# Performance work log

Hardware: AMD Instinct MI355X
Metric: run time of the kernel (lower is better)

## Reference

```python
import jax, jax.numpy as jnp
import numpy as np

B, S, D = 4, 2048, 1024  # batch, seq_len, input_dim == output_dim (dk)


def setup_inputs() -> dict:
    key = jax.random.key(0)
    kx, kq, kk, kv = jax.random.split(key, 4)
    # xavier_uniform bound for square [D, D] matrices
    bound = float(np.sqrt(6.0 / (D + D)))
    return {
        "x": jax.random.normal(kx, (B, S, D), dtype=jnp.float32),
        "WQ": jax.random.uniform(kq, (D, D), jnp.float32, -bound, bound),
        "WK": jax.random.uniform(kk, (D, D), jnp.float32, -bound, bound),
        "WV": jax.random.uniform(kv, (D, D), jnp.float32, -bound, bound),
    }


def reference(x, WQ, WK, WV):
    dk = WQ.shape[1]
    q = x @ WQ  # [B, S, dk]
    k = x @ WK
    v = x @ WV
    scores = jnp.einsum("bsd,btd->bst", q, k) / jnp.sqrt(jnp.asarray(dk, x.dtype))
    # causal mask: tril ones -> positions where mask==0 set to -inf
    s = x.shape[1]
    causal = jnp.tril(jnp.ones((s, s), dtype=bool))
    scores = jnp.where(causal[None, :, :], scores, jnp.asarray(-jnp.inf, x.dtype))
    attention = jax.nn.softmax(scores, axis=-1)
    # NOTE: original applies attention_dropout to `scores` post-softmax and
    # discards the result -> dead op; eval-mode output is attention @ v.
    return jnp.einsum("bst,btd->bsd", attention, v)
```

## Files before the change

kernel.cpp:

```cpp
#include <hip/hip_runtime.h>
#include <stdint.h>


typedef unsigned short u16;
typedef __attribute__((ext_vector_type(8))) short shortx8;
typedef __attribute__((ext_vector_type(4))) float floatx4;

static constexpr int BB = 4;
static constexpr int SS = 2048;
static constexpr int DD = 1024;

__device__ __forceinline__ u16 f2bf(float f) {
  union { float f; uint32_t u; } c; c.f = f;
  uint32_t u = c.u;
  return (u16)((u + 0x7fffu + ((u >> 16) & 1u)) >> 16);
}

__device__ __forceinline__ float bfhi2f(uint32_t u) {
  union { uint32_t u; float f; } c; c.u = u & 0xffff0000u; return c.f;
}
__device__ __forceinline__ float bflo2f(uint32_t u) {
  union { uint32_t u; float f; } c; c.u = u << 16; return c.f;
}

#define GLOAD_LDS16(g_, l_)                                                             \
  __builtin_amdgcn_global_load_lds((const __attribute__((address_space(1))) void*)(g_), \
                                   (__attribute__((address_space(3))) void*)(l_), 16, 0, 0)

__device__ __forceinline__ void gemm_core_128(
    const u16* __restrict__ A, const u16* __restrict__ Bt,
    int lda, int ldb, int m0, int n0, int kend, floatx4 acc[4][4])
{
  __shared__ u16 lA[128 * 64];
  __shared__ u16 lB[128 * 64];
  const int t = threadIdx.x;
  const int w = t >> 6, l = t & 63;
  const int wm = w >> 1, wn = w & 1;
  const int sr = l >> 3;
  const int scq = ((l & 7) ^ (l >> 3)) * 8;

#pragma unroll
  for (int i = 0; i < 4; ++i)
#pragma unroll
    for (int j = 0; j < 4; ++j)
      acc[i][j] = (floatx4){0.f, 0.f, 0.f, 0.f};

  const u16* Ab = A + (size_t)m0 * lda;
  const u16* Bb = Bt + (size_t)n0 * ldb;

  for (int k0 = 0; k0 < kend; k0 += 64) {
#pragma unroll
    for (int i = 0; i < 4; ++i) {
      const int row = w * 32 + i * 8;
      GLOAD_LDS16(Ab + (size_t)(row + sr) * lda + k0 + scq, &lA[row * 64]);
      GLOAD_LDS16(Bb + (size_t)(row + sr) * ldb + k0 + scq, &lB[row * 64]);
    }
    __syncthreads();

#pragma unroll
    for (int ks = 0; ks < 2; ++ks) {
      const int ca = ((ks * 4 + (l >> 4)) ^ (l & 7)) * 8;
      shortx8 af[4], bf[4];
#pragma unroll
      for (int i = 0; i < 4; ++i)
        af[i] = *(const shortx8*)&lA[(wm * 64 + i * 16 + (l & 15)) * 64 + ca];
#pragma unroll
      for (int i = 0; i < 4; ++i)
        bf[i] = *(const shortx8*)&lB[(wn * 64 + i * 16 + (l & 15)) * 64 + ca];
#pragma unroll
      for (int i = 0; i < 4; ++i)
#pragma unroll
        for (int j = 0; j < 4; ++j)
          acc[i][j] = __builtin_amdgcn_mfma_f32_16x16x32_bf16(af[i], bf[j], acc[i][j], 0, 0, 0);
    }
    __syncthreads();
  }
}

#define LOAD_AF(mh_)                                                                     \
  _Pragma("unroll")                                                                      \
  for (int mi = 0; mi < 4; ++mi)                                                         \
    _Pragma("unroll")                                                                    \
    for (int kk = 0; kk < 2; ++kk)                                                       \
      af[mi][kk] = *(const shortx8*)&As[((mh_) * 128 + wr * 64 + mi * 16 + fr) * 64 +    \
                                        (((kk * 4 + fq) ^ (l & 7)) * 8)];

#define LOAD_BF(nh_)                                                                     \
  _Pragma("unroll")                                                                      \
  for (int ni = 0; ni < 2; ++ni)                                                         \
    _Pragma("unroll")                                                                    \
    for (int kk = 0; kk < 2; ++kk)                                                       \
      bf[ni][kk] = *(const shortx8*)&Bs[((nh_) * 128 + wc * 32 + ni * 16 + fr) * 64 +    \
                                        (((kk * 4 + fq) ^ (l & 7)) * 8)];

#define MFMA_QUAD(mh_, nh_)                                                              \
  do {                                                                                   \
    __builtin_amdgcn_s_setprio(1);                                                       \
    _Pragma("unroll")                                                                    \
    for (int mi = 0; mi < 4; ++mi)                                                       \
      _Pragma("unroll")                                                                  \
      for (int ni = 0; ni < 2; ++ni)                                                     \
        _Pragma("unroll")                                                                \
        for (int kk = 0; kk < 2; ++kk)                                                   \
          acc[mh_][nh_][mi][ni] = __builtin_amdgcn_mfma_f32_16x16x32_bf16(               \
              af[mi][kk], bf[ni][kk], acc[mh_][nh_][mi][ni], 0, 0, 0);                   \
    __builtin_amdgcn_s_setprio(0);                                                       \
  } while (0)

#define STAGE_A(buf_, half_, k_)                                                         \
  do {                                                                                   \
    _Pragma("unroll")                                                                    \
    for (int j = 0; j < 2; ++j) {                                                        \
      const int row0 = (half_) * 128 + wv * 16 + j * 8;                                  \
      GLOAD_LDS16(Ab + (size_t)(row0 + sr) * lda + (k_) + scq, &sm[buf_][0][row0 * 64]); \
    }                                                                                    \
  } while (0)

#define STAGE_B(buf_, half_, k_)                                                         \
  do {                                                                                   \
    _Pragma("unroll")                                                                    \
    for (int j = 0; j < 2; ++j) {                                                        \
      const int row0 = (half_) * 128 + wv * 16 + j * 8;                                  \
      GLOAD_LDS16(Bb + (size_t)(row0 + sr) * ldb + (k_) + scq, &sm[buf_][1][row0 * 64]); \
    }                                                                                    \
  } while (0)

__device__ __forceinline__ void gemm_core_256(
    const u16* __restrict__ A, const u16* __restrict__ Bt,
    int lda, int ldb, int m0, int n0, int kend,
    floatx4 (&acc)[2][2][4][2])
{
  __shared__ u16 sm[2][2][256 * 64];
  const int t = threadIdx.x;
  const int wv = t >> 6, l = t & 63;
  const int wr = wv >> 2, wc = wv & 3;
  const int fr = l & 15, fq = l >> 4;
  const int sr = l >> 3;
  const int scq = ((l & 7) ^ sr) * 8;

#pragma unroll
  for (int a = 0; a < 2; ++a)
#pragma unroll
    for (int bq = 0; bq < 2; ++bq)
#pragma unroll
      for (int mi = 0; mi < 4; ++mi)
#pragma unroll
        for (int ni = 0; ni < 2; ++ni)
          acc[a][bq][mi][ni] = (floatx4){0.f, 0.f, 0.f, 0.f};

  const u16* Ab = A + (size_t)m0 * lda;
  const u16* Bb = Bt + (size_t)n0 * ldb;
  const int T = kend >> 6;

  STAGE_A(0, 0, 0); STAGE_A(0, 1, 0);
  STAGE_B(0, 0, 0); STAGE_B(0, 1, 0);
  {
    const int k1p = (T > 1) ? 64 : 0;
    STAGE_A(1, 0, k1p);
    STAGE_B(1, 1, k1p);
  }
  asm volatile("s_waitcnt vmcnt(4)" ::: "memory");
  __builtin_amdgcn_s_barrier();

  shortx8 af[4][2], bf[2][2];

  for (int tt = 0; tt < T; ++tt) {
    const int c = tt & 1, o = c ^ 1;
    const u16* As = &sm[c][0][0];
    const u16* Bs = &sm[c][1][0];
    const int kn1 = ((tt + 1 < T) ? tt + 1 : T - 1) * 64;
    const int kn2 = ((tt + 2 < T) ? tt + 2 : T - 1) * 64;

    LOAD_AF(0); LOAD_BF(0);
    STAGE_A(o, 1, kn1);
    __builtin_amdgcn_s_barrier();
    asm volatile("s_waitcnt lgkmcnt(0)" ::: "memory");
    MFMA_QUAD(0, 0);
    __builtin_amdgcn_s_barrier();

    LOAD_BF(1);
    STAGE_B(o, 0, kn1);
    __builtin_amdgcn_s_barrier();
    asm volatile("s_waitcnt lgkmcnt(0)" ::: "memory");
    MFMA_QUAD(0, 1);
    __builtin_amdgcn_s_barrier();

    LOAD_AF(1);
    STAGE_A(c, 0, kn2);
    __builtin_amdgcn_s_barrier();
    asm volatile("s_waitcnt lgkmcnt(0)" ::: "memory");
    MFMA_QUAD(1, 1);
    __builtin_amdgcn_s_barrier();

    LOAD_BF(0);
    STAGE_B(c, 1, kn2);
    __builtin_amdgcn_s_barrier();
    asm volatile("s_waitcnt lgkmcnt(0)" ::: "memory");
    MFMA_QUAD(1, 0);
    asm volatile("s_waitcnt vmcnt(4)" ::: "memory");
    __builtin_amdgcn_s_barrier();
  }
  asm volatile("s_waitcnt vmcnt(0)" ::: "memory");
}

__global__ __launch_bounds__(256) void prep(const float* __restrict__ x,
                                            const float* __restrict__ WQ,
                                            const float* __restrict__ WK,
                                            const float* __restrict__ WV,
                                            u16* __restrict__ xb,
                                            u16* __restrict__ Wt) {
  __shared__ float tile[64][65];
  const int bid = blockIdx.x;
  const int t = threadIdx.x;
  if (bid < 8192) {
    const size_t i = (size_t)bid * 256 + t;
    float4 v = ((const float4*)x)[i];
    ushort4 o;
    o.x = f2bf(v.x); o.y = f2bf(v.y); o.z = f2bf(v.z); o.w = f2bf(v.w);
    ((ushort4*)xb)[i] = o;
    return;
  }
  const int r = bid - 8192;
  const int wsel = r >> 8;
  const int rr = r & 255;
  const int k0 = (rr >> 4) * 64, n0 = (rr & 15) * 64;
  const float* W = wsel == 0 ? WQ : (wsel == 1 ? WK : WV);
  const int tx = t & 63, ty = t >> 6;
#pragma unroll
  for (int i = 0; i < 16; ++i)
    tile[ty + i * 4][tx] = W[(size_t)(k0 + ty + i * 4) * DD + n0 + tx];
  __syncthreads();
  u16* dst = Wt + (size_t)wsel * DD * DD;
#pragma unroll
  for (int i = 0; i < 16; ++i)
    dst[(size_t)(n0 + ty + i * 4) * DD + k0 + tx] = f2bf(tile[tx][ty + i * 4]);
}

__global__ __launch_bounds__(512, 2) void qkv_gemm(const u16* __restrict__ x,
                                                   const u16* __restrict__ Wt,
                                                   u16* __restrict__ Q,
                                                   u16* __restrict__ K,
                                                   u16* __restrict__ Vt) {
  const int m0 = blockIdx.x * 256;
  const int n0t = blockIdx.y * 256;
  floatx4 acc[2][2][4][2];
  gemm_core_256(x, Wt, DD, DD, m0, n0t, DD, acc);

  const int t = threadIdx.x, wv = t >> 6, l = t & 63;
  const int wr = wv >> 2, wc = wv & 3;
  const int fr = l & 15, fq = l >> 4;

  if (n0t >= 2048) {
    const int bb = m0 >> 11;
    u16* vt = Vt + (size_t)bb * DD * SS;
    const int sb = m0 & 2047;
#pragma unroll
    for (int mh = 0; mh < 2; ++mh)
#pragma unroll
      for (int nh = 0; nh < 2; ++nh)
#pragma unroll
        for (int mi = 0; mi < 4; ++mi)
#pragma unroll
          for (int ni = 0; ni < 2; ++ni) {
            const int d = (n0t - 2048) + nh * 128 + wc * 32 + ni * 16 + fr;
            const int s = sb + mh * 128 + wr * 64 + mi * 16 + fq * 4;
            ushort4 o4;
            o4.x = f2bf(acc[mh][nh][mi][ni][0]);
            o4.y = f2bf(acc[mh][nh][mi][ni][1]);
            o4.z = f2bf(acc[mh][nh][mi][ni][2]);
            o4.w = f2bf(acc[mh][nh][mi][ni][3]);
            *(ushort4*)(vt + (size_t)d * SS + s) = o4;
          }
    return;
  }

  u16* out = (n0t < 1024) ? Q : K;
  const int n0 = n0t & 1023;
#pragma unroll
  for (int mh = 0; mh < 2; ++mh)
#pragma unroll
    for (int nh = 0; nh < 2; ++nh)
#pragma unroll
      for (int mi = 0; mi < 4; ++mi)
#pragma unroll
        for (int ni = 0; ni < 2; ++ni)
#pragma unroll
          for (int r = 0; r < 4; ++r) {
            const int m = m0 + mh * 128 + wr * 64 + mi * 16 + fq * 4 + r;
            const int n = n0 + nh * 128 + wc * 32 + ni * 16 + fr;
            out[(size_t)m * DD + n] = f2bf(acc[mh][nh][mi][ni][r]);
          }
}

__global__ __launch_bounds__(512, 2) void scores_gemm(const u16* __restrict__ Q,
                                                      const u16* __restrict__ Kt,
                                                      u16* __restrict__ Scb) {
  const int b = blockIdx.z;
  const int tcode = blockIdx.x;
  int mb = (int)((sqrtf(8.0f * (float)tcode + 1.0f) - 1.0f) * 0.5f);
  while ((mb + 1) * (mb + 2) / 2 <= tcode) ++mb;
  while (mb * (mb + 1) / 2 > tcode) --mb;
  const int nb = tcode - mb * (mb + 1) / 2;
  const int m0 = mb * 256, n0 = nb * 256;

  floatx4 acc[2][2][4][2];
  gemm_core_256(Q + (size_t)b * SS * DD, Kt + (size_t)b * SS * DD, DD, DD, m0, n0, DD, acc);

  u16* out = Scb + (size_t)b * SS * SS;
  const int t = threadIdx.x, wv = t >> 6, l = t & 63;
  const int wr = wv >> 2, wc = wv & 3;
  const int fr = l & 15, fq = l >> 4;
#pragma unroll
  for (int mh = 0; mh < 2; ++mh)
#pragma unroll
    for (int nh = 0; nh < 2; ++nh)
#pragma unroll
      for (int mi = 0; mi < 4; ++mi)
#pragma unroll
        for (int ni = 0; ni < 2; ++ni)
#pragma unroll
          for (int r = 0; r < 4; ++r) {
            const int m = m0 + mh * 128 + wr * 64 + mi * 16 + fq * 4 + r;
            const int n = n0 + nh * 128 + wc * 32 + ni * 16 + fr;
            out[(size_t)m * SS + n] = f2bf(acc[mh][nh][mi][ni][r] * 0.03125f);
          }
}

__global__ __launch_bounds__(256) void softmax_causal(const u16* __restrict__ Scb,
                                                      u16* __restrict__ P) {
  const int row = blockIdx.x * 4 + (threadIdx.x >> 6);
  const int l = threadIdx.x & 63;
  const int b = row >> 11, i = row & 2047;
  const u16* s = Scb + (size_t)b * SS * SS + (size_t)i * SS;
  u16* p = P + (size_t)b * SS * SS + (size_t)i * SS;
  const int n = i + 1;
  const int jend = (i + 128) & ~127;
  const int nc = (jend + 511) >> 9;

  float v[4][8];
  float mx = -INFINITY;
#pragma unroll
  for (int c = 0; c < 4; ++c) {
    if (c < nc) {
      const int col = c * 512 + l * 8;
      uint4 raw = *(const uint4*)(s + col);
      v[c][0] = bflo2f(raw.x); v[c][1] = bfhi2f(raw.x);
      v[c][2] = bflo2f(raw.y); v[c][3] = bfhi2f(raw.y);
      v[c][4] = bflo2f(raw.z); v[c][5] = bfhi2f(raw.z);
      v[c][6] = bflo2f(raw.w); v[c][7] = bfhi2f(raw.w);
#pragma unroll
      for (int e = 0; e < 8; ++e) {
        v[c][e] = (col + e < n) ? v[c][e] : -INFINITY;
        mx = fmaxf(mx, v[c][e]);
      }
    }
  }
#pragma unroll
  for (int o = 32; o > 0; o >>= 1) mx = fmaxf(mx, __shfl_xor(mx, o, 64));

  float sum = 0.f;
#pragma unroll
  for (int c = 0; c < 4; ++c) {
    if (c < nc) {
#pragma unroll
      for (int e = 0; e < 8; ++e) {
        v[c][e] = __expf(v[c][e] - mx);
        sum += v[c][e];
      }
    }
  }
#pragma unroll
  for (int o = 32; o > 0; o >>= 1) sum += __shfl_xor(sum, o, 64);
  const float inv = 1.0f / sum;

#pragma unroll
  for (int c = 0; c < 4; ++c) {
    if (c < nc) {
      const int col = c * 512 + l * 8;
      if (col < jend) {
        uint4 o4;
        o4.x = (uint32_t)f2bf(v[c][0] * inv) | ((uint32_t)f2bf(v[c][1] * inv) << 16);
        o4.y = (uint32_t)f2bf(v[c][2] * inv) | ((uint32_t)f2bf(v[c][3] * inv) << 16);
        o4.z = (uint32_t)f2bf(v[c][4] * inv) | ((uint32_t)f2bf(v[c][5] * inv) << 16);
        o4.w = (uint32_t)f2bf(v[c][6] * inv) | ((uint32_t)f2bf(v[c][7] * inv) << 16);
        *(uint4*)(p + col) = o4;
      }
    }
  }
}

__global__ __launch_bounds__(256, 2) void pv_gemm(const u16* __restrict__ P,
                                                  const u16* __restrict__ Vt,
                                                  float* __restrict__ out) {
  const int b = blockIdx.z;
  const int mb = 15 - blockIdx.y;
  const int m0 = mb * 128, n0 = blockIdx.x * 128;
  floatx4 acc[4][4];
  gemm_core_128(P + (size_t)b * SS * SS, Vt + (size_t)b * DD * SS, SS, SS, m0, n0, m0 + 128, acc);

  float* o = out + (size_t)b * SS * DD;
  const int t = threadIdx.x, w = t >> 6, l = t & 63;
  const int wm = w >> 1, wn = w & 1;
#pragma unroll
  for (int i = 0; i < 4; ++i)
#pragma unroll
    for (int j = 0; j < 4; ++j)
#pragma unroll
      for (int r = 0; r < 4; ++r) {
        const int m = m0 + wm * 64 + i * 16 + (l >> 4) * 4 + r;
        const int n = n0 + wn * 64 + j * 16 + (l & 15);
        o[(size_t)m * DD + n] = acc[i][j][r];
      }
}

extern "C" void kernel_launch(void* const* d_in, const int* in_sizes, int n_in,
                              void* d_out, int out_size, void* d_ws, size_t ws_size,
                              hipStream_t stream) {
  const float* x  = (const float*)d_in[0];
  const float* WQ = (const float*)d_in[1];
  const float* WK = (const float*)d_in[2];
  const float* WV = (const float*)d_in[3];
  float* out = (float*)d_out;

  char* ws = (char*)d_ws;
  const size_t WT_OFF = 0;
  const size_t XB_OFF = WT_OFF + (size_t)3072 * 1024 * 2;
  const size_t Q_OFF  = XB_OFF + (size_t)BB * SS * DD * 2;
  const size_t K_OFF  = Q_OFF + (size_t)BB * SS * DD * 2;
  const size_t VT_OFF = K_OFF + (size_t)BB * SS * DD * 2;
  const size_t P_OFF  = VT_OFF + (size_t)BB * SS * DD * 2;
  const size_t SC_OFF = P_OFF + (size_t)BB * SS * SS * 2;
  u16* Wt  = (u16*)(ws + WT_OFF);
  u16* xb  = (u16*)(ws + XB_OFF);
  u16* Q   = (u16*)(ws + Q_OFF);
  u16* Kb  = (u16*)(ws + K_OFF);
  u16* Vt  = (u16*)(ws + VT_OFF);
  u16* P   = (u16*)(ws + P_OFF);
  u16* Scb = (u16*)(ws + SC_OFF);

  hipLaunchKernelGGL(prep, dim3(8960), dim3(256), 0, stream, x, WQ, WK, WV, xb, Wt);
  hipLaunchKernelGGL(qkv_gemm, dim3(32, 12), dim3(512), 0, stream, xb, Wt, Q, Kb, Vt);
  hipLaunchKernelGGL(scores_gemm, dim3(36, 1, 4), dim3(512), 0, stream, Q, Kb, Scb);
  hipLaunchKernelGGL(softmax_causal, dim3(2048), dim3(256), 0, stream, Scb, P);
  hipLaunchKernelGGL(pv_gemm, dim3(8, 16, 4), dim3(256), 0, stream, P, Vt, out);
}
```

Before: 239.8 us.

## Unroll GEMM K-loop by two and keep both B fragment halves in registers

The 256-tile GEMM main loop is unrolled two K-steps per iteration with fixed buffer indices. It keeps two B fragment register sets so the fourth MFMA quad reuses bf0 instead of reloading it from LDS. The staging order of the next tiles is reshuffled so one LDS reload and barrier phase per K-step disappears. This costs more VGPRs and assumes T is even. The waitcnt counts were retuned by hand, which risks races if the counts are wrong.

```diff
diff --git a/kernel.cpp b/kernel.cpp
--- a/kernel.cpp
+++ b/kernel.cpp
@@ -77,23 +77,23 @@
   }
 }
 
-#define LOAD_AF(mh_)                                                                     \
+#define LOAD_AF(buf_, mh_)                                                               \
   _Pragma("unroll")                                                                      \
   for (int mi = 0; mi < 4; ++mi)                                                         \
     _Pragma("unroll")                                                                    \
     for (int kk = 0; kk < 2; ++kk)                                                       \
-      af[mi][kk] = *(const shortx8*)&As[((mh_) * 128 + wr * 64 + mi * 16 + fr) * 64 +    \
-                                        (((kk * 4 + fq) ^ (l & 7)) * 8)];
-
-#define LOAD_BF(nh_)                                                                     \
+      af[mi][kk] = *(const shortx8*)&sm[buf_][0][((mh_) * 128 + wr * 64 + mi * 16 + fr) * 64 + \
+                                                 (((kk * 4 + fq) ^ (l & 7)) * 8)];
+
+#define LOAD_BF(dst_, buf_, nh_)                                                         \
   _Pragma("unroll")                                                                      \
   for (int ni = 0; ni < 2; ++ni)                                                         \
     _Pragma("unroll")                                                                    \
     for (int kk = 0; kk < 2; ++kk)                                                       \
-      bf[ni][kk] = *(const shortx8*)&Bs[((nh_) * 128 + wc * 32 + ni * 16 + fr) * 64 +    \
-                                        (((kk * 4 + fq) ^ (l & 7)) * 8)];
-
-#define MFMA_QUAD(mh_, nh_)                                                              \
+      dst_[ni][kk] = *(const shortx8*)&sm[buf_][1][((nh_) * 128 + wc * 32 + ni * 16 + fr) * 64 + \
+                                                   (((kk * 4 + fq) ^ (l & 7)) * 8)];
+
+#define MFMA_QUAD(mh_, nh_, b_)                                                          \
   do {                                                                                   \
     __builtin_amdgcn_s_setprio(1);                                                       \
     _Pragma("unroll")                                                                    \
@@ -103,7 +103,7 @@
         _Pragma("unroll")                                                                \
         for (int kk = 0; kk < 2; ++kk)                                                   \
           acc[mh_][nh_][mi][ni] = __builtin_amdgcn_mfma_f32_16x16x32_bf16(               \
-              af[mi][kk], bf[ni][kk], acc[mh_][nh_][mi][ni], 0, 0, 0);                   \
+              af[mi][kk], b_[ni][kk], acc[mh_][nh_][mi][ni], 0, 0, 0);                   \
     __builtin_amdgcn_s_setprio(0);                                                       \
   } while (0)
 
@@ -124,6 +124,12 @@
       GLOAD_LDS16(Bb + (size_t)(row0 + sr) * ldb + (k_) + scq, &sm[buf_][1][row0 * 64]); \
     }                                                                                    \
   } while (0)
+
+#define PH_SYNC_MFMA(mh_, nh_, b_)                                                       \
+  __builtin_amdgcn_s_barrier();                                                          \
+  asm volatile("s_waitcnt lgkmcnt(0)" ::: "memory");                                     \
+  MFMA_QUAD(mh_, nh_, b_);                                                               \
+  __builtin_amdgcn_s_barrier();
 
 __device__ __forceinline__ void gemm_core_256(
     const u16* __restrict__ A, const u16* __restrict__ Bt,
@@ -151,52 +157,58 @@
   const u16* Ab = A + (size_t)m0 * lda;
   const u16* Bb = Bt + (size_t)n0 * ldb;
   const int T = kend >> 6;
+  const int NI = T >> 1;
 
   STAGE_A(0, 0, 0); STAGE_A(0, 1, 0);
   STAGE_B(0, 0, 0); STAGE_B(0, 1, 0);
-  {
-    const int k1p = (T > 1) ? 64 : 0;
-    STAGE_A(1, 0, k1p);
-    STAGE_B(1, 1, k1p);
-  }
-  asm volatile("s_waitcnt vmcnt(4)" ::: "memory");
+  STAGE_B(1, 0, 64);
+  STAGE_A(1, 0, 64);
+  STAGE_B(1, 1, 64);
+  asm volatile("s_waitcnt vmcnt(6)" ::: "memory");
   __builtin_amdgcn_s_barrier();
 
-  shortx8 af[4][2], bf[2][2];
-
-  for (int tt = 0; tt < T; ++tt) {
-    const int c = tt & 1, o = c ^ 1;
-    const u16* As = &sm[c][0][0];
-    const u16* Bs = &sm[c][1][0];
-    const int kn1 = ((tt + 1 < T) ? tt + 1 : T - 1) * 64;
-    const int kn2 = ((tt + 2 < T) ? tt + 2 : T - 1) * 64;
-
-    LOAD_AF(0); LOAD_BF(0);
-    STAGE_A(o, 1, kn1);
+  shortx8 af[4][2], bf0[2][2], bf1[2][2];
+
+  for (int it = 0; it < NI; ++it) {
+    const int t0 = it * 2;
+    const int k1 = (t0 + 1) * 64;
+    const int kA = ((t0 + 2 < T) ? t0 + 2 : T - 1) * 64;
+    const int kB = ((t0 + 3 < T) ? t0 + 3 : T - 1) * 64;
+    LOAD_AF(0, 0); LOAD_BF(bf0, 0, 0);
+    STAGE_A(1, 1, k1);
+    asm volatile("s_waitcnt lgkmcnt(8)" ::: "memory");
+    PH_SYNC_MFMA(0, 0, bf0);
+
+    LOAD_BF(bf1, 0, 1);
+    STAGE_B(0, 0, kA);
+    PH_SYNC_MFMA(0, 1, bf1);
+
+    LOAD_AF(0, 1);
+    STAGE_A(0, 0, kA);
+    PH_SYNC_MFMA(1, 1, bf1);
+
+    STAGE_B(0, 1, kA);
     __builtin_amdgcn_s_barrier();
-    asm volatile("s_waitcnt lgkmcnt(0)" ::: "memory");
-    MFMA_QUAD(0, 0);
+    MFMA_QUAD(1, 0, bf0);
+    asm volatile("s_waitcnt vmcnt(4)" ::: "memory");
     __builtin_amdgcn_s_barrier();
 
-    LOAD_BF(1);
-    STAGE_B(o, 0, kn1);
+    LOAD_AF(1, 0); LOAD_BF(bf0, 1, 0);
+    STAGE_A(0, 1, kA);
+    asm volatile("s_waitcnt lgkmcnt(8)" ::: "memory");
+    PH_SYNC_MFMA(0, 0, bf0);
+
+    LOAD_BF(bf1, 1, 1);
+    STAGE_B(1, 0, kB);
+    PH_SYNC_MFMA(0, 1, bf1);
+
+    LOAD_AF(1, 1);
+    STAGE_A(1, 0, kB);
+    PH_SYNC_MFMA(1, 1, bf1);
+
+    STAGE_B(1, 1, kB);
     __builtin_amdgcn_s_barrier();
-    asm volatile("s_waitcnt lgkmcnt(0)" ::: "memory");
-    MFMA_QUAD(0, 1);
-    __builtin_amdgcn_s_barrier();
-
-    LOAD_AF(1);
-    STAGE_A(c, 0, kn2);
-    __builtin_amdgcn_s_barrier();
-    asm volatile("s_waitcnt lgkmcnt(0)" ::: "memory");
-    MFMA_QUAD(1, 1);
-    __builtin_amdgcn_s_barrier();
-
-    LOAD_BF(0);
-    STAGE_B(c, 1, kn2);
-    __builtin_amdgcn_s_barrier();
-    asm volatile("s_waitcnt lgkmcnt(0)" ::: "memory");
-    MFMA_QUAD(1, 0);
+    MFMA_QUAD(1, 0, bf0);
     asm volatile("s_waitcnt vmcnt(4)" ::: "memory");
     __builtin_amdgcn_s_barrier();
   }
```

After: 249.5 us. 1.04x slower.
